# Kernel optimization log

Hardware: AMD Instinct MI355X
Metric: run time of the kernel (lower is better)

The kernel has to match this reference:

```python
import jax, jax.numpy as jnp
import numpy as np

B, S, H, DH = 2, 4096, 8, 64
D = H * DH


def setup_inputs() -> dict:
    key = jax.random.key(0)
    ks = jax.random.split(key, 6)
    std = 1.0 / np.sqrt(D)
    return {
        "x": jax.random.normal(ks[0], (B, S, D), dtype=jnp.float32),
        "Wq": jax.random.normal(ks[1], (D, D), dtype=jnp.float32) * std,
        "Wk": jax.random.normal(ks[2], (D, D), dtype=jnp.float32) * std,
        "Wv": jax.random.normal(ks[3], (D, D), dtype=jnp.float32) * std,
        "Wo": jax.random.normal(ks[4], (D, D), dtype=jnp.float32) * std,
        "bo": jnp.zeros((D,), dtype=jnp.float32),
    }


def reference(x, Wq, Wk, Wv, Wo, bo):
    scale = DH ** (-0.5)
    # torch Linear: y = x @ W.T
    q = x @ Wq.T  # [B,S,D]
    k = x @ Wk.T
    v = x @ Wv.T
    # split heads -> [B,H,S,Dh]
    q = q.reshape(B, S, H, DH).transpose(0, 2, 1, 3)
    k = k.reshape(B, S, H, DH).transpose(0, 2, 1, 3)
    v = v.reshape(B, S, H, DH).transpose(0, 2, 1, 3)
    score = jnp.einsum('bhqd,bhkd->bhqk', q, k) * scale  # [B,H,S,S]
    weights = jax.nn.softmax(score, axis=-1)
    attn = jnp.einsum('bhqk,bhkd->bhqd', weights, v)  # [B,H,S,Dh]
    h_ = attn.transpose(0, 2, 1, 3).reshape(B, S, D)
    return h_ @ Wo.T + bo
```

## Files before the change

kernel.cpp:

```cpp
#include <hip/hip_runtime.h>

#define LOG2E 1.44269504088896340736f

typedef unsigned short u16;
typedef short s16x4 __attribute__((ext_vector_type(4)));
typedef __bf16 bf16x4_t __attribute__((ext_vector_type(4)));
typedef __bf16 bf16x8_t __attribute__((ext_vector_type(8)));
typedef float f32x4_t __attribute__((ext_vector_type(4)));

__device__ __forceinline__ u16 f2bf(float f) {
  union { float f; unsigned int u; } v;
  v.f = f;
  unsigned int u = v.u;
  u += 0x7fffu + ((u >> 16) & 1u);
  return (u16)(u >> 16);
}

__device__ __forceinline__ f32x4_t mfma16(bf16x8_t a, bf16x8_t b, f32x4_t c) {
  return __builtin_amdgcn_mfma_f32_16x16x32_bf16(a, b, c, 0, 0, 0);
}
__device__ __forceinline__ f32x4_t mfma16x16(s16x4 a, s16x4 b, f32x4_t c) {
  return __builtin_amdgcn_mfma_f32_16x16x16bf16_1k(a, b, c, 0, 0, 0);
}

__device__ __forceinline__ void gl_lds16(const u16* g, u16* l) {
  __builtin_amdgcn_global_load_lds(
      (const __attribute__((address_space(1))) unsigned int*)g,
      (__attribute__((address_space(3))) unsigned int*)l, 16, 0, 0);
}

__global__ __launch_bounds__(256) void cast_all_kernel(
    const float* __restrict__ x, const float* __restrict__ wq, const float* __restrict__ wk,
    const float* __restrict__ wv, const float* __restrict__ wo,
    u16* __restrict__ xb, u16* __restrict__ wqb, u16* __restrict__ wkb,
    u16* __restrict__ wvb, u16* __restrict__ wob) {
  const int NX = 2 * 4096 * 512;
  const int NW = 512 * 512;
  int i = (blockIdx.x * 256 + threadIdx.x) * 4;
  const float* src; u16* dst; int off; float scale = 1.f;
  if (i < NX)               { src = x;  dst = xb;  off = i; }
  else if (i < NX + NW)     { src = wq; dst = wqb; off = i - NX; scale = 0.125f * LOG2E; }
  else if (i < NX + 2 * NW) { src = wk; dst = wkb; off = i - NX - NW; }
  else if (i < NX + 3 * NW) { src = wv; dst = wvb; off = i - NX - 2 * NW; }
  else                      { src = wo; dst = wob; off = i - NX - 3 * NW; }
  float4 f = *(const float4*)(src + off);
  unsigned int lo = (unsigned int)f2bf(f.x * scale) | ((unsigned int)f2bf(f.y * scale) << 16);
  unsigned int hi = (unsigned int)f2bf(f.z * scale) | ((unsigned int)f2bf(f.w * scale) << 16);
  uint2 o; o.x = lo; o.y = hi;
  *(uint2*)(dst + off) = o;
}

template <int MODE>
__device__ __forceinline__ void gemm_core(const u16* __restrict__ A, const u16* __restrict__ Bt,
                                          void* __restrict__ Cout, const float* __restrict__ bias,
                                          int Mbase, int Nbase) {
  __shared__ __align__(16) u16 As[128][40];
  __shared__ __align__(16) u16 Bs[128][40];
  const int t = threadIdx.x;
  const int wave = t >> 6, lane = t & 63;
  const int r = lane & 15, qd = lane >> 4;
  const int wm = wave & 1, wn = wave >> 1;
  const int lr = t >> 2;
  const int lc = (t & 3) * 8;

  f32x4_t acc[4][4];
#pragma unroll
  for (int i = 0; i < 4; i++)
#pragma unroll
    for (int j = 0; j < 4; j++) { f32x4_t z = {0.f, 0.f, 0.f, 0.f}; acc[i][j] = z; }

  const u16* pa0 = A  + (Mbase + lr) * 512 + lc;
  const u16* pa1 = A  + (Mbase + 64 + lr) * 512 + lc;
  const u16* pb0 = Bt + (Nbase + lr) * 512 + lc;
  const u16* pb1 = Bt + (Nbase + 64 + lr) * 512 + lc;

  uint4 ra0 = *(const uint4*)(pa0);
  uint4 ra1 = *(const uint4*)(pa1);
  uint4 rb0 = *(const uint4*)(pb0);
  uint4 rb1 = *(const uint4*)(pb1);

  for (int k0 = 0; k0 < 512; k0 += 32) {
    *(uint4*)&As[lr][lc]      = ra0;
    *(uint4*)&As[64 + lr][lc] = ra1;
    *(uint4*)&Bs[lr][lc]      = rb0;
    *(uint4*)&Bs[64 + lr][lc] = rb1;
    __syncthreads();
    if (k0 < 480) {
      ra0 = *(const uint4*)(pa0 + k0 + 32);
      ra1 = *(const uint4*)(pa1 + k0 + 32);
      rb0 = *(const uint4*)(pb0 + k0 + 32);
      rb1 = *(const uint4*)(pb1 + k0 + 32);
    }
    bf16x8_t af[4], bfr[4];
#pragma unroll
    for (int i = 0; i < 4; i++) af[i]  = *(const bf16x8_t*)&As[wm * 64 + i * 16 + r][qd * 8];
#pragma unroll
    for (int j = 0; j < 4; j++) bfr[j] = *(const bf16x8_t*)&Bs[wn * 64 + j * 16 + r][qd * 8];
#pragma unroll
    for (int i = 0; i < 4; i++)
#pragma unroll
      for (int j = 0; j < 4; j++) acc[i][j] = mfma16(af[i], bfr[j], acc[i][j]);
    __syncthreads();
  }

  float bv[4];
  if (MODE == 2) {
#pragma unroll
    for (int j = 0; j < 4; j++) bv[j] = bias[Nbase + wn * 64 + j * 16 + r];
  }
#pragma unroll
  for (int i = 0; i < 4; i++) {
#pragma unroll
    for (int reg = 0; reg < 4; reg++) {
      int gr = Mbase + wm * 64 + i * 16 + qd * 4 + reg;
#pragma unroll
      for (int j = 0; j < 4; j++) {
        int gc = Nbase + wn * 64 + j * 16 + r;
        float val = acc[i][j][reg];
        if (MODE == 2) {
          ((float*)Cout)[gr * 512 + gc] = val + bv[j];
        } else if (MODE == 1) {
          int bb = gc >> 12, ss = gc & 4095;
          ((__bf16*)Cout)[((long)(bb * 512 + gr)) * 4096 + ss] = (__bf16)val;
        } else {
          ((__bf16*)Cout)[gr * 512 + gc] = (__bf16)val;
        }
      }
    }
  }
}

__global__ __launch_bounds__(256) void gemm_qkv_kernel(
    const u16* __restrict__ X,
    const u16* __restrict__ Wq, const u16* __restrict__ Wk, const u16* __restrict__ Wv,
    u16* __restrict__ Q, u16* __restrict__ K, u16* __restrict__ Vt) {
  if (blockIdx.z == 0)
    gemm_core<0>(X, Wq, Q, nullptr, blockIdx.x * 128, blockIdx.y * 128);
  else if (blockIdx.z == 1)
    gemm_core<0>(X, Wk, K, nullptr, blockIdx.x * 128, blockIdx.y * 128);
  else
    gemm_core<1>(Wv, X, Vt, nullptr, blockIdx.y * 128, blockIdx.x * 128);
}

__global__ __launch_bounds__(256) void gemm_out_kernel(
    const u16* __restrict__ Aat, const u16* __restrict__ Wo,
    float* __restrict__ Out, const float* __restrict__ bo) {
  gemm_core<2>(Aat, Wo, Out, bo, blockIdx.x * 128, blockIdx.y * 128);
}

__global__ __launch_bounds__(256, 2) void attn_kernel(
    const u16* __restrict__ Q, const u16* __restrict__ K, const u16* __restrict__ Vt,
    u16* __restrict__ Oattn) {
  __shared__ __align__(16) u16 Ks[2][2][4096];
  __shared__ __align__(16) u16 Vs[2][2][4096];

  const int t = threadIdx.x;
  const int wave = t >> 6, lane = t & 63;
  const int r = lane & 15, qd = lane >> 4;
  const int g = wave & 1, kv = wave >> 1;
  const int bh = blockIdx.y;
  const int b = bh >> 3, h = bh & 7;
  const long bbase = (long)b * 4096 * 512;
  const int q0 = blockIdx.x * 128;

  const int sw = r & 7;
  const int ck0 = (qd ^ sw) * 8;
  const int ck1 = ((qd + 4) ^ sw) * 8;
  int vck[4];
#pragma unroll
  for (int ks = 0; ks < 4; ks++)
    vck[ks] = ((ks * 2 + (qd >> 1)) ^ sw) * 8 + (qd & 1) * 4;

  bf16x8_t qf[4][2];
#pragma unroll
  for (int qa = 0; qa < 4; qa++) {
    const u16* qp = Q + bbase + (long)(q0 + g * 64 + qa * 16 + r) * 512 + h * 64 + qd * 8;
    qf[qa][0] = *(const bf16x8_t*)(qp);
    qf[qa][1] = *(const bf16x8_t*)(qp + 32);
  }

  f32x4_t accO[4][4];
  float Lacc[4];
#pragma unroll
  for (int qa = 0; qa < 4; qa++) {
    f32x4_t z = {0.f, 0.f, 0.f, 0.f};
    Lacc[qa] = 0.f;
#pragma unroll
    for (int nt = 0; nt < 4; nt++) accO[qa][nt] = z;
  }

  const int rr = lane >> 3;
  const int cc = (lane & 7) ^ rr;
  const u16* kgb = K + bbase + (long)(kv * 2048 + g * 32 + rr) * 512 + h * 64 + cc * 8;
  const u16* vgb = Vt + ((long)(b * 512 + h * 64 + g * 32 + rr)) * 4096 + kv * 2048 + cc * 8;

#pragma unroll
  for (int i = 0; i < 4; i++) gl_lds16(kgb + (long)i * 8 * 512, &Ks[kv][0][g * 2048] + i * 512);
#pragma unroll
  for (int i = 0; i < 4; i++) gl_lds16(vgb + i * 8 * 4096, &Vs[kv][0][g * 2048] + i * 512);

  for (int it = 0; it < 32; it++) {
    const int buf = it & 1;
    __syncthreads();

    if (it < 31) {
      const int nb = (it + 1) & 1;
      const long ko = (long)(it + 1) * 64;
#pragma unroll
      for (int i = 0; i < 4; i++)
        gl_lds16(kgb + (ko + i * 8) * 512, &Ks[kv][nb][g * 2048] + i * 512);
#pragma unroll
      for (int i = 0; i < 4; i++)
        gl_lds16(vgb + ko + (long)i * 8 * 4096, &Vs[kv][nb][g * 2048] + i * 512);
    }

    bf16x8_t kf[4][2];
#pragma unroll
    for (int nt = 0; nt < 4; nt++) {
      const u16* kb = &Ks[kv][buf][(nt * 16 + r) * 64];
      kf[nt][0] = *(const bf16x8_t*)(kb + ck0);
      kf[nt][1] = *(const bf16x8_t*)(kb + ck1);
    }

    f32x4_t St[4][4];
#pragma unroll
    for (int qa = 0; qa < 4; qa++)
#pragma unroll
      for (int nt = 0; nt < 4; nt++) {
        f32x4_t z = {0.f, 0.f, 0.f, 0.f};
        z = mfma16(kf[nt][0], qf[qa][0], z);
        z = mfma16(kf[nt][1], qf[qa][1], z);
        St[qa][nt] = z;
      }

    s16x4 pk[4][4];
#pragma unroll
    for (int qa = 0; qa < 4; qa++)
#pragma unroll
      for (int nt = 0; nt < 4; nt++) {
        float p0 = __builtin_amdgcn_exp2f(St[qa][nt][0]);
        float p1 = __builtin_amdgcn_exp2f(St[qa][nt][1]);
        float p2 = __builtin_amdgcn_exp2f(St[qa][nt][2]);
        float p3 = __builtin_amdgcn_exp2f(St[qa][nt][3]);
        Lacc[qa] += (p0 + p1) + (p2 + p3);
        bf16x4_t pb;
        pb[0] = (__bf16)p0; pb[1] = (__bf16)p1; pb[2] = (__bf16)p2; pb[3] = (__bf16)p3;
        pk[qa][nt] = *(s16x4*)&pb;
      }

#pragma unroll
    for (int ks = 0; ks < 4; ks++) {
      s16x4 va[4];
#pragma unroll
      for (int dm = 0; dm < 4; dm++)
        va[dm] = *(const s16x4*)&Vs[kv][buf][(dm * 16 + r) * 64 + vck[ks]];
#pragma unroll
      for (int qa = 0; qa < 4; qa++)
#pragma unroll
        for (int dm = 0; dm < 4; dm++)
          accO[qa][dm] = mfma16x16(va[dm], pk[qa][ks], accO[qa][dm]);
    }
  }

  __syncthreads();
  float* Sc  = (float*)&Ks[0][0][0];
  float* Lsc = (float*)&Vs[0][0][0];
  if (kv == 1) {
#pragma unroll
    for (int qa = 0; qa < 4; qa++) {
#pragma unroll
      for (int dm = 0; dm < 4; dm++)
        *(f32x4_t*)&Sc[g * 4096 + ((qa * 4 + dm) * 64 + lane) * 4] = accO[qa][dm];
      Lsc[g * 256 + qa * 64 + lane] = Lacc[qa];
    }
  }
  __syncthreads();
  if (kv == 0) {
#pragma unroll
    for (int qa = 0; qa < 4; qa++) {
      Lacc[qa] += Lsc[g * 256 + qa * 64 + lane];
      float v = Lacc[qa];
      v += __shfl_xor(v, 16);
      v += __shfl_xor(v, 32);
      Lacc[qa] = v;
    }
#pragma unroll
    for (int qa = 0; qa < 4; qa++) {
      float inv = 1.f / Lacc[qa];
      int gq = q0 + g * 64 + qa * 16 + r;
#pragma unroll
      for (int dm = 0; dm < 4; dm++) {
        f32x4_t o = *(const f32x4_t*)&Sc[g * 4096 + ((qa * 4 + dm) * 64 + lane) * 4];
        o += accO[qa][dm];
        bf16x4_t ob;
#pragma unroll
        for (int reg = 0; reg < 4; reg++) ob[reg] = (__bf16)(o[reg] * inv);
        *(uint2*)&Oattn[bbase + (long)gq * 512 + h * 64 + dm * 16 + qd * 4] = *(uint2*)&ob;
      }
    }
  }
}

extern "C" void kernel_launch(void* const* d_in, const int* in_sizes, int n_in,
                              void* d_out, int out_size, void* d_ws, size_t ws_size,
                              hipStream_t stream) {
  const float* x  = (const float*)d_in[0];
  const float* Wq = (const float*)d_in[1];
  const float* Wk = (const float*)d_in[2];
  const float* Wv = (const float*)d_in[3];
  const float* Wo = (const float*)d_in[4];
  const float* bo = (const float*)d_in[5];
  float* out = (float*)d_out;

  u16* ws  = (u16*)d_ws;
  u16* xb  = ws;
  u16* wqb = xb  + 4194304;
  u16* wkb = wqb + 262144;
  u16* wvb = wkb + 262144;
  u16* wob = wvb + 262144;
  u16* Qb  = wob + 262144;
  u16* Kb  = Qb  + 4194304;
  u16* Vtg = Kb  + 4194304;
  u16* Ab  = Vtg + 4194304;

  cast_all_kernel<<<5120, 256, 0, stream>>>(x, Wq, Wk, Wv, Wo, xb, wqb, wkb, wvb, wob);

  dim3 g1(64, 4, 3);
  gemm_qkv_kernel<<<g1, 256, 0, stream>>>(xb, wqb, wkb, wvb, Qb, Kb, Vtg);

  dim3 g2(32, 16);
  attn_kernel<<<g2, 256, 0, stream>>>(Qb, Kb, Vtg, Ab);

  dim3 g3(64, 4);
  gemm_out_kernel<<<g3, 256, 0, stream>>>(Ab, wob, out, bo);
}
```

Before: 197.1 us.

## Double-buffer GEMM via direct global-to-LDS loads and compute softmax sums with MFMA

The projection GEMM core switches from register-staged single-buffer LDS tiles with K-step 32 to double-buffered LDS tiles with K-step 64. Tiles are filled by direct global-to-LDS loads using an XOR swizzle, and each step now needs one barrier instead of two. The attention kernel drops the per-lane VALU accumulation of softmax row sums and the cross-lane shuffles. Instead it accumulates the sums by running MFMAs of the bf16 probabilities against a ones vector, and converts to bf16 with a vector convert. This uses more LDS and adds MFMA work, and the row sums are now taken from the bf16-rounded probabilities.

```diff
diff --git a/kernel.cpp b/kernel.cpp
--- a/kernel.cpp
+++ b/kernel.cpp
@@ -54,14 +54,21 @@
 __device__ __forceinline__ void gemm_core(const u16* __restrict__ A, const u16* __restrict__ Bt,
                                           void* __restrict__ Cout, const float* __restrict__ bias,
                                           int Mbase, int Nbase) {
-  __shared__ __align__(16) u16 As[128][40];
-  __shared__ __align__(16) u16 Bs[128][40];
+  __shared__ __align__(16) u16 As[2][128 * 64];
+  __shared__ __align__(16) u16 Bs[2][128 * 64];
   const int t = threadIdx.x;
   const int wave = t >> 6, lane = t & 63;
   const int r = lane & 15, qd = lane >> 4;
   const int wm = wave & 1, wn = wave >> 1;
-  const int lr = t >> 2;
-  const int lc = (t & 3) * 8;
+
+  const int rr = lane >> 3;
+  const int cc = (lane & 7) ^ rr;
+  const u16* pa = A  + (Mbase + wave * 32 + rr) * 512 + cc * 8;
+  const u16* pb = Bt + (Nbase + wave * 32 + rr) * 512 + cc * 8;
+
+  const int sw = r & 7;
+  const int ck0 = (qd ^ sw) * 8;
+  const int ck1 = ((qd + 4) ^ sw) * 8;
 
   f32x4_t acc[4][4];
 #pragma unroll
@@ -69,38 +76,44 @@
 #pragma unroll
     for (int j = 0; j < 4; j++) { f32x4_t z = {0.f, 0.f, 0.f, 0.f}; acc[i][j] = z; }
 
-  const u16* pa0 = A  + (Mbase + lr) * 512 + lc;
-  const u16* pa1 = A  + (Mbase + 64 + lr) * 512 + lc;
-  const u16* pb0 = Bt + (Nbase + lr) * 512 + lc;
-  const u16* pb1 = Bt + (Nbase + 64 + lr) * 512 + lc;
-
-  uint4 ra0 = *(const uint4*)(pa0);
-  uint4 ra1 = *(const uint4*)(pa1);
-  uint4 rb0 = *(const uint4*)(pb0);
-  uint4 rb1 = *(const uint4*)(pb1);
-
-  for (int k0 = 0; k0 < 512; k0 += 32) {
-    *(uint4*)&As[lr][lc]      = ra0;
-    *(uint4*)&As[64 + lr][lc] = ra1;
-    *(uint4*)&Bs[lr][lc]      = rb0;
-    *(uint4*)&Bs[64 + lr][lc] = rb1;
+#pragma unroll
+  for (int i = 0; i < 4; i++) {
+    gl_lds16(pa + i * 8 * 512, &As[0][(wave * 32 + i * 8) * 64]);
+    gl_lds16(pb + i * 8 * 512, &Bs[0][(wave * 32 + i * 8) * 64]);
+  }
+
+  for (int it = 0; it < 8; it++) {
+    const int buf = it & 1;
     __syncthreads();
-    if (k0 < 480) {
-      ra0 = *(const uint4*)(pa0 + k0 + 32);
-      ra1 = *(const uint4*)(pa1 + k0 + 32);
-      rb0 = *(const uint4*)(pb0 + k0 + 32);
-      rb1 = *(const uint4*)(pb1 + k0 + 32);
-    }
-    bf16x8_t af[4], bfr[4];
-#pragma unroll
-    for (int i = 0; i < 4; i++) af[i]  = *(const bf16x8_t*)&As[wm * 64 + i * 16 + r][qd * 8];
-#pragma unroll
-    for (int j = 0; j < 4; j++) bfr[j] = *(const bf16x8_t*)&Bs[wn * 64 + j * 16 + r][qd * 8];
-#pragma unroll
-    for (int i = 0; i < 4; i++)
-#pragma unroll
-      for (int j = 0; j < 4; j++) acc[i][j] = mfma16(af[i], bfr[j], acc[i][j]);
-    __syncthreads();
+    if (it < 7) {
+      const int nb = buf ^ 1;
+      const int ko = (it + 1) * 64;
+#pragma unroll
+      for (int i = 0; i < 4; i++) {
+        gl_lds16(pa + ko + i * 8 * 512, &As[nb][(wave * 32 + i * 8) * 64]);
+        gl_lds16(pb + ko + i * 8 * 512, &Bs[nb][(wave * 32 + i * 8) * 64]);
+      }
+    }
+    bf16x8_t af[2][4], bfr[2][4];
+#pragma unroll
+    for (int i = 0; i < 4; i++) {
+      const u16* ab = &As[buf][(wm * 64 + i * 16 + r) * 64];
+      af[0][i] = *(const bf16x8_t*)(ab + ck0);
+      af[1][i] = *(const bf16x8_t*)(ab + ck1);
+    }
+#pragma unroll
+    for (int j = 0; j < 4; j++) {
+      const u16* bb = &Bs[buf][(wn * 64 + j * 16 + r) * 64];
+      bfr[0][j] = *(const bf16x8_t*)(bb + ck0);
+      bfr[1][j] = *(const bf16x8_t*)(bb + ck1);
+    }
+#pragma unroll
+    for (int kh = 0; kh < 2; kh++)
+#pragma unroll
+      for (int i = 0; i < 4; i++)
+#pragma unroll
+        for (int j = 0; j < 4; j++)
+          acc[i][j] = mfma16(af[kh][i], bfr[kh][j], acc[i][j]);
   }
 
   float bv[4];
@@ -171,6 +184,10 @@
   for (int ks = 0; ks < 4; ks++)
     vck[ks] = ((ks * 2 + (qd >> 1)) ^ sw) * 8 + (qd & 1) * 4;
 
+  s16x4 ones;
+#pragma unroll
+  for (int j = 0; j < 4; j++) ones[j] = (short)0x3F80;
+
   bf16x8_t qf[4][2];
 #pragma unroll
   for (int qa = 0; qa < 4; qa++) {
@@ -180,11 +197,11 @@
   }
 
   f32x4_t accO[4][4];
-  float Lacc[4];
+  f32x4_t accL[4];
 #pragma unroll
   for (int qa = 0; qa < 4; qa++) {
     f32x4_t z = {0.f, 0.f, 0.f, 0.f};
-    Lacc[qa] = 0.f;
+    accL[qa] = z;
 #pragma unroll
     for (int nt = 0; nt < 4; nt++) accO[qa][nt] = z;
   }
@@ -238,15 +255,20 @@
     for (int qa = 0; qa < 4; qa++)
 #pragma unroll
       for (int nt = 0; nt < 4; nt++) {
-        float p0 = __builtin_amdgcn_exp2f(St[qa][nt][0]);
-        float p1 = __builtin_amdgcn_exp2f(St[qa][nt][1]);
-        float p2 = __builtin_amdgcn_exp2f(St[qa][nt][2]);
-        float p3 = __builtin_amdgcn_exp2f(St[qa][nt][3]);
-        Lacc[qa] += (p0 + p1) + (p2 + p3);
-        bf16x4_t pb;
-        pb[0] = (__bf16)p0; pb[1] = (__bf16)p1; pb[2] = (__bf16)p2; pb[3] = (__bf16)p3;
+        f32x4_t pe;
+        pe[0] = __builtin_amdgcn_exp2f(St[qa][nt][0]);
+        pe[1] = __builtin_amdgcn_exp2f(St[qa][nt][1]);
+        pe[2] = __builtin_amdgcn_exp2f(St[qa][nt][2]);
+        pe[3] = __builtin_amdgcn_exp2f(St[qa][nt][3]);
+        bf16x4_t pb = __builtin_convertvector(pe, bf16x4_t);
         pk[qa][nt] = *(s16x4*)&pb;
       }
+
+#pragma unroll
+    for (int qa = 0; qa < 4; qa++)
+#pragma unroll
+      for (int ks = 0; ks < 4; ks++)
+        accL[qa] = mfma16x16(ones, pk[qa][ks], accL[qa]);
 
 #pragma unroll
     for (int ks = 0; ks < 4; ks++) {
@@ -271,22 +293,15 @@
 #pragma unroll
       for (int dm = 0; dm < 4; dm++)
         *(f32x4_t*)&Sc[g * 4096 + ((qa * 4 + dm) * 64 + lane) * 4] = accO[qa][dm];
-      Lsc[g * 256 + qa * 64 + lane] = Lacc[qa];
+      Lsc[g * 256 + qa * 64 + lane] = accL[qa][0];
     }
   }
   __syncthreads();
   if (kv == 0) {
 #pragma unroll
     for (int qa = 0; qa < 4; qa++) {
-      Lacc[qa] += Lsc[g * 256 + qa * 64 + lane];
-      float v = Lacc[qa];
-      v += __shfl_xor(v, 16);
-      v += __shfl_xor(v, 32);
-      Lacc[qa] = v;
-    }
-#pragma unroll
-    for (int qa = 0; qa < 4; qa++) {
-      float inv = 1.f / Lacc[qa];
+      float L = accL[qa][0] + Lsc[g * 256 + qa * 64 + lane];
+      float inv = 1.f / L;
       int gq = q0 + g * 64 + qa * 16 + r;
 #pragma unroll
       for (int dm = 0; dm < 4; dm++) {
```

After: 210.0 us. +6.5%, slower.

## Use 16x16x32 MFMA for PV and compute softmax row sums via MFMA with ones

Applied to the files above, without the earlier changes.

Replaces the 16x16x16 bf16 MFMAs in the P·V product with the 16x16x32 variant, which halves the number of PV MFMA instructions. P is packed into bf16x8 fragments, and V fragments are assembled from two 8-byte LDS reads. The per-lane exp sum accumulation and the end-of-kernel shuffle reduction are replaced by MFMAs against a vector of ones. The row sum is now taken from the bf16-rounded probabilities, which matches the PV numerator, and it adds 8 extra MFMAs per iteration.

```diff
diff --git a/kernel.cpp b/kernel.cpp
--- a/kernel.cpp
+++ b/kernel.cpp
@@ -3,7 +3,6 @@
 #define LOG2E 1.44269504088896340736f
 
 typedef unsigned short u16;
-typedef short s16x4 __attribute__((ext_vector_type(4)));
 typedef __bf16 bf16x4_t __attribute__((ext_vector_type(4)));
 typedef __bf16 bf16x8_t __attribute__((ext_vector_type(8)));
 typedef float f32x4_t __attribute__((ext_vector_type(4)));
@@ -18,9 +17,6 @@
 
 __device__ __forceinline__ f32x4_t mfma16(bf16x8_t a, bf16x8_t b, f32x4_t c) {
   return __builtin_amdgcn_mfma_f32_16x16x32_bf16(a, b, c, 0, 0, 0);
-}
-__device__ __forceinline__ f32x4_t mfma16x16(s16x4 a, s16x4 b, f32x4_t c) {
-  return __builtin_amdgcn_mfma_f32_16x16x16bf16_1k(a, b, c, 0, 0, 0);
 }
 
 __device__ __forceinline__ void gl_lds16(const u16* g, u16* l) {
@@ -166,10 +162,16 @@
   const int sw = r & 7;
   const int ck0 = (qd ^ sw) * 8;
   const int ck1 = ((qd + 4) ^ sw) * 8;
-  int vck[4];
-#pragma unroll
-  for (int ks = 0; ks < 4; ks++)
-    vck[ks] = ((ks * 2 + (qd >> 1)) ^ sw) * 8 + (qd & 1) * 4;
+  int vo0[2], vo1[2];
+#pragma unroll
+  for (int c = 0; c < 2; c++) {
+    vo0[c] = ((c * 4 + (qd >> 1)) ^ sw) * 8 + 4 * (qd & 1);
+    vo1[c] = ((c * 4 + 2 + (qd >> 1)) ^ sw) * 8 + 4 * (qd & 1);
+  }
+
+  bf16x8_t ones8;
+#pragma unroll
+  for (int j = 0; j < 8; j++) ones8[j] = (__bf16)1.0f;
 
   bf16x8_t qf[4][2];
 #pragma unroll
@@ -180,11 +182,11 @@
   }
 
   f32x4_t accO[4][4];
-  float Lacc[4];
+  f32x4_t accL[4];
 #pragma unroll
   for (int qa = 0; qa < 4; qa++) {
     f32x4_t z = {0.f, 0.f, 0.f, 0.f};
-    Lacc[qa] = 0.f;
+    accL[qa] = z;
 #pragma unroll
     for (int nt = 0; nt < 4; nt++) accO[qa][nt] = z;
   }
@@ -233,32 +235,47 @@
         St[qa][nt] = z;
       }
 
-    s16x4 pk[4][4];
+    bf16x8_t pf[4][2];
 #pragma unroll
     for (int qa = 0; qa < 4; qa++)
 #pragma unroll
-      for (int nt = 0; nt < 4; nt++) {
-        float p0 = __builtin_amdgcn_exp2f(St[qa][nt][0]);
-        float p1 = __builtin_amdgcn_exp2f(St[qa][nt][1]);
-        float p2 = __builtin_amdgcn_exp2f(St[qa][nt][2]);
-        float p3 = __builtin_amdgcn_exp2f(St[qa][nt][3]);
-        Lacc[qa] += (p0 + p1) + (p2 + p3);
-        bf16x4_t pb;
-        pb[0] = (__bf16)p0; pb[1] = (__bf16)p1; pb[2] = (__bf16)p2; pb[3] = (__bf16)p3;
-        pk[qa][nt] = *(s16x4*)&pb;
-      }
-
-#pragma unroll
-    for (int ks = 0; ks < 4; ks++) {
-      s16x4 va[4];
-#pragma unroll
-      for (int dm = 0; dm < 4; dm++)
-        va[dm] = *(const s16x4*)&Vs[kv][buf][(dm * 16 + r) * 64 + vck[ks]];
+      for (int c = 0; c < 2; c++) {
+        f32x4_t e0, e1;
+#pragma unroll
+        for (int j = 0; j < 4; j++) {
+          e0[j] = __builtin_amdgcn_exp2f(St[qa][2 * c][j]);
+          e1[j] = __builtin_amdgcn_exp2f(St[qa][2 * c + 1][j]);
+        }
+        bf16x4_t b0 = __builtin_convertvector(e0, bf16x4_t);
+        bf16x4_t b1 = __builtin_convertvector(e1, bf16x4_t);
+        bf16x8_t p8;
+#pragma unroll
+        for (int j = 0; j < 4; j++) { p8[j] = b0[j]; p8[4 + j] = b1[j]; }
+        pf[qa][c] = p8;
+      }
+
+#pragma unroll
+    for (int qa = 0; qa < 4; qa++)
+#pragma unroll
+      for (int c = 0; c < 2; c++)
+        accL[qa] = mfma16(ones8, pf[qa][c], accL[qa]);
+
+#pragma unroll
+    for (int c = 0; c < 2; c++) {
+      bf16x8_t va[4];
+#pragma unroll
+      for (int dm = 0; dm < 4; dm++) {
+        const u16* vb = &Vs[kv][buf][(dm * 16 + r) * 64];
+        union { uint4 u; bf16x8_t v; } cat;
+        *(uint2*)&cat.u.x = *(const uint2*)(vb + vo0[c]);
+        *(uint2*)&cat.u.z = *(const uint2*)(vb + vo1[c]);
+        va[dm] = cat.v;
+      }
 #pragma unroll
       for (int qa = 0; qa < 4; qa++)
 #pragma unroll
         for (int dm = 0; dm < 4; dm++)
-          accO[qa][dm] = mfma16x16(va[dm], pk[qa][ks], accO[qa][dm]);
+          accO[qa][dm] = mfma16(va[dm], pf[qa][c], accO[qa][dm]);
     }
   }
 
@@ -271,22 +288,15 @@
 #pragma unroll
       for (int dm = 0; dm < 4; dm++)
         *(f32x4_t*)&Sc[g * 4096 + ((qa * 4 + dm) * 64 + lane) * 4] = accO[qa][dm];
-      Lsc[g * 256 + qa * 64 + lane] = Lacc[qa];
+      Lsc[g * 256 + qa * 64 + lane] = accL[qa][0];
     }
   }
   __syncthreads();
   if (kv == 0) {
 #pragma unroll
     for (int qa = 0; qa < 4; qa++) {
-      Lacc[qa] += Lsc[g * 256 + qa * 64 + lane];
-      float v = Lacc[qa];
-      v += __shfl_xor(v, 16);
-      v += __shfl_xor(v, 32);
-      Lacc[qa] = v;
-    }
-#pragma unroll
-    for (int qa = 0; qa < 4; qa++) {
-      float inv = 1.f / Lacc[qa];
+      float L = accL[qa][0] + Lsc[g * 256 + qa * 64 + lane];
+      float inv = 1.f / L;
       int gq = q0 + g * 64 + qa * 16 + r;
 #pragma unroll
       for (int dm = 0; dm < 4; dm++) {
```

New measurement: 191.9 us. 2.6% less time.
